# Kernel optimization log

Hardware: AMD Instinct MI355X
Metric: run time of the kernel (lower is better)

The kernel has to match this reference:

```python
import jax, jax.numpy as jnp
import numpy as np

B, CIN, W = 4, 3, 28          # batch, in_channels, image size (= max_pos_embedding)
MID, HEADS, G, COUT = 16, 8, 4, 64
HALF = MID // 2               # row / col embedding dims


def _embed(u, w1, b1, gamma, beta, w2, b2):
    """Positional-embedding MLP applied elementwise to scalars u (N,).
    Conv2d(1->16,k=1) -> LayerNorm(16 channels) -> Swish -> Conv2d(16->MID/2,k=1)."""
    h = u[:, None] * w1[None, :] + b1                     # (N, 16)
    mu = h.mean(-1, keepdims=True)
    var = ((h - mu) ** 2).mean(-1, keepdims=True)
    h = gamma * (h - mu) / jnp.sqrt(var + 1e-5) + beta    # LayerNorm over channels
    h = h * jax.nn.sigmoid(h)                             # Swish
    return h @ w2.T + b2                                  # (N, HALF)


def _rot_indices():
    """Acted relative-position lookup indices for the 4 rotations.
    Values index into u = concat(rel, -rel) where rel = linspace(-1,1,2W-1)."""
    n = 2 * W - 1
    ar = np.arange(W)
    rel = ar[None, :] - ar[:, None] + (W - 1)             # rel[i,k] in [0, 2W-2]
    R = np.broadcast_to(rel[:, None, :, None], (W,) * 4)  # depends on (i,k)
    C = np.broadcast_to(rel[None, :, None, :], (W,) * 4)  # depends on (j,l)
    # rotation by 0/90/180/270 deg acting on (row, col) relative coordinates
    ridx = np.stack([R, C + n, R + n, C], 0)              # row component index
    cidx = np.stack([C, R, C + n, R + n], 0)              # col component index
    return jnp.asarray(ridx, jnp.int32), jnp.asarray(cidx, jnp.int32)


def setup_inputs() -> dict:
    key = jax.random.key(0)
    ks = jax.random.split(key, 24)
    def nrm(k, shape, fan):
        return jax.random.normal(k, shape, jnp.float32) / np.float32(np.sqrt(fan))
    inp = {"x": jax.random.normal(ks[0], (B, CIN, W, W), jnp.float32)}
    inp["wq"] = nrm(ks[1], (MID * HEADS, CIN), CIN); inp["bq"] = jnp.zeros((MID * HEADS,), jnp.float32)
    inp["wk"] = nrm(ks[2], (MID * HEADS, CIN), CIN); inp["bk"] = jnp.zeros((MID * HEADS,), jnp.float32)
    inp["wv"] = nrm(ks[3], (MID * HEADS, CIN), CIN); inp["bv"] = jnp.zeros((MID * HEADS,), jnp.float32)
    inp["w_out"] = nrm(ks[4], (COUT, MID * HEADS), MID * HEADS); inp["b_out"] = jnp.zeros((COUT,), jnp.float32)
    for pfx, base in (("row", 5), ("col", 12)):
        inp[f"{pfx}_w1"] = nrm(ks[base], (16,), 1)
        inp[f"{pfx}_b1"] = jnp.zeros((16,), jnp.float32)
        inp[f"{pfx}_gamma"] = jnp.ones((16,), jnp.float32)
        inp[f"{pfx}_beta"] = jnp.zeros((16,), jnp.float32)
        inp[f"{pfx}_w2"] = nrm(ks[base + 1], (HALF, 16), 16)
        inp[f"{pfx}_b2"] = jnp.zeros((HALF,), jnp.float32)
    inp["ridx"], inp["cidx"] = _rot_indices()
    return inp


def reference(x, wq, bq, wk, bk, wv, bv, w_out, b_out,
              row_w1, row_b1, row_gamma, row_beta, row_w2, row_b2,
              col_w1, col_b1, col_gamma, col_beta, col_w2, col_b2,
              ridx, cidx):
    b, c, H, Wd = x.shape
    # 1x1-conv q/k/v, viewed as (b, mid, heads, H, W)
    q = (jnp.einsum('oc,bcij->boij', wq, x) + bq[:, None, None]).reshape(b, MID, HEADS, H, Wd)
    k_ = (jnp.einsum('oc,bcij->boij', wk, x) + bk[:, None, None]).reshape(b, MID, HEADS, H, Wd)
    v = (jnp.einsum('oc,bcij->boij', wv, x) + bv[:, None, None]).reshape(b, MID, HEADS, H, Wd)

    content = jnp.einsum('bmhij,bmhkl->bhijkl', q, k_)     # (b,h,i,j,k,l)

    lin = jnp.linspace(-1.0, 1.0, 2 * Wd - 1)
    u = jnp.concatenate([lin, -lin])                       # unique relative coords
    E_row = _embed(u, row_w1, row_b1, row_gamma, row_beta, row_w2, row_b2)
    E_col = _embed(u, col_w1, col_b1, col_gamma, col_beta, col_w2, col_b2)
    row_emb = E_row[ridx]                                  # (G,i,j,k,l,HALF)
    col_emb = E_col[cidx]

    scores = jnp.einsum('bmhij,gijklm->bhgijkl', q[:, :HALF], row_emb)
    scores = scores + jnp.einsum('bmhij,gijklm->bhgijkl', q[:, HALF:], col_emb)
    scores = (scores + content[:, :, None]) / np.float32(np.sqrt(c))

    sh = scores.shape                                      # softmax over flattened (k,l)
    probs = jax.nn.softmax(scores.reshape(sh[:-2] + (-1,)), axis=-1).reshape(sh)

    out_v = jnp.einsum('bhgijkl,bmhkl->bmhgij', probs, v)  # (b,mid,heads,G,i,j)
    out_v = out_v.reshape(b, MID * HEADS, G, H, Wd)
    out = jnp.einsum('om,bmgij->bogij', w_out, out_v) + b_out[:, None, None, None]
    return out
```

## Files before the change

kernel.cpp:

```cpp
#include <hip/hip_runtime.h>
#include <hip/hip_fp16.h>

#define NPOS 784
#define WDIM 28

typedef _Float16 f16x8 __attribute__((ext_vector_type(8)));
typedef _Float16 f16x4 __attribute__((ext_vector_type(4)));
typedef float    f32x4 __attribute__((ext_vector_type(4)));

__global__ __launch_bounds__(256) void prep_kernel(
    const float* __restrict__ x,
    const float* __restrict__ wk, const float* __restrict__ bk,
    const float* __restrict__ wv, const float* __restrict__ bv,
    const float* __restrict__ w_out,
    const float* __restrict__ rw1, const float* __restrict__ rb1,
    const float* __restrict__ rga, const float* __restrict__ rbe,
    const float* __restrict__ rw2, const float* __restrict__ rb2,
    const float* __restrict__ cw1, const float* __restrict__ cb1,
    const float* __restrict__ cga, const float* __restrict__ cbe,
    const float* __restrict__ cw2, const float* __restrict__ cb2,
    _Float16* __restrict__ Kfrag, _Float16* __restrict__ Vfrag,
    _Float16* __restrict__ Wfrag,
    float* __restrict__ Etr, float* __restrict__ Etc)
{
    const int t = threadIdx.x;
    if (blockIdx.x == 416) {
        int d = -1;
        const float *w1 = rw1, *b1 = rb1, *ga = rga, *be = rbe, *w2 = rw2, *b2 = rb2;
        float* E = Etr;
        if (t < 110) { d = t; }
        else if (t >= 128 && t < 238) { d = t - 128; w1 = cw1; b1 = cb1; ga = cga; be = cbe; w2 = cw2; b2 = cb2; E = Etc; }
        if (d < 0) return;
        float u = (d < 55) ? (-1.0f + (float)d * (2.0f / 54.0f))
                           : -(-1.0f + (float)(d - 55) * (2.0f / 54.0f));
        float hb[16], mu = 0.0f;
#pragma unroll
        for (int c = 0; c < 16; ++c) { hb[c] = u * w1[c] + b1[c]; mu += hb[c]; }
        mu *= (1.0f / 16.0f);
        float var = 0.0f;
#pragma unroll
        for (int c = 0; c < 16; ++c) { float dv = hb[c] - mu; var += dv * dv; }
        var *= (1.0f / 16.0f);
        float rstd = rsqrtf(var + 1e-5f);
#pragma unroll
        for (int c = 0; c < 16; ++c) {
            float hn = ga[c] * (hb[c] - mu) * rstd + be[c];
            hb[c] = hn / (1.0f + __expf(-hn));
        }
#pragma unroll
        for (int m = 0; m < 8; ++m) {
            float e = b2[m];
#pragma unroll
            for (int c = 0; c < 16; ++c) e += hb[c] * w2[m * 16 + c];
            E[m * 110 + d] = e;
        }
        return;
    }
    if (blockIdx.x == 417) {
        for (int idx = t; idx < 8192; idx += 256) {
            int obc = idx >> 9, lane = (idx >> 3) & 63, j = idx & 7;
            int o  = (obc >> 2) * 16 + (lane & 15);
            int mh = (obc & 3) * 32 + (lane >> 4) * 8 + j;
            Wfrag[idx] = (_Float16)w_out[o * 128 + mh];
        }
        return;
    }

    const int bid  = blockIdx.x;
    const int b    = bid / 104, rem = bid - b * 104;
    const int tile = rem >> 3, h = rem & 7;
    const int lane = t & 63, mg = t >> 6;
    const int bh   = b * 8 + h;

    {
        if (t < 128) {
            int sub = (t >> 5) & 3, l32 = 32 + (t & 31);
            int qz = tile * 4 + sub;
            if (qz < 49)
                *(f16x8*)(Kfrag + ((size_t)(bh * 49 + qz) * 64 + l32) * 8) = (f16x8){};
        }
        if (tile == 12 && t < 32)
            *(f16x8*)(Vfrag + ((size_t)(bh * 25 + 24) * 64 + 32 + t) * 8) = (f16x8){};
    }

    const int ij = tile * 64 + lane;
    if (ij >= NPOS) return;

    float x0 = x[(b * 3 + 0) * NPOS + ij];
    float x1 = x[(b * 3 + 1) * NPOS + ij];
    float x2 = x[(b * 3 + 2) * NPOS + ij];

    float4 kv;
    float vv[4];
#pragma unroll
    for (int j = 0; j < 4; ++j) {
        int m = mg * 4 + j, oc = m * 8 + h;
        float w0, w1, w2v;
        w0 = wk[oc*3+0]; w1 = wk[oc*3+1]; w2v = wk[oc*3+2];
        ((float*)&kv)[j] = bk[oc] + w0*x0 + w1*x1 + w2v*x2;
        w0 = wv[oc*3+0]; w1 = wv[oc*3+1]; w2v = wv[oc*3+2];
        vv[j] = bv[oc] + w0*x0 + w1*x1 + w2v*x2;
    }
    {
        int qt = ij >> 4;
        int lp = ((mg >> 1) << 4) | (ij & 15);
        int jb = (mg & 1) * 4;
        f16x4 k4 = {(_Float16)kv.x, (_Float16)kv.y, (_Float16)kv.z, (_Float16)kv.w};
        *(f16x4*)(Kfrag + ((size_t)(bh * 49 + qt) * 64 + lp) * 8 + jb) = k4;
    }
    {
        int s5 = ij >> 5, kk = ij & 31;
        _Float16* vb = Vfrag + (((size_t)(bh * 25 + s5) * 64 + ((kk >> 3) << 4)) << 3) + (kk & 7);
#pragma unroll
        for (int j = 0; j < 4; ++j) vb[(mg * 4 + j) * 8] = (_Float16)vv[j];
    }
}

#define UNI_OFF 56320
#define MX_OFF  97280
#define PS_OFF  98304
__global__ __launch_bounds__(1024, 1) void attn_kernel(
    const _Float16* __restrict__ Kfrag, const _Float16* __restrict__ Vfrag,
    const _Float16* __restrict__ Wfrag,
    const float* __restrict__ Etr, const float* __restrict__ Etc,
    const float* __restrict__ x,
    const float* __restrict__ wq, const float* __restrict__ bq,
    const float* __restrict__ b_out, float* __restrict__ out)
{
    __shared__ __align__(16) unsigned char smem[100352];
    const int t = threadIdx.x, wave = t >> 6, lane = t & 63;
    const int q15 = lane & 15, rg = lane >> 4;
    const int h = wave & 7, hf = wave >> 3;

    int bid = blockIdx.x;
    int xcd = bid & 7;
    int lb  = ((xcd < 4) ? xcd * 25 : 100 + (xcd - 4) * 24) + (bid >> 3);
    const int b = lb / 49, qt = lb - b * 49;
    const int bh = b * 8 + h;
    const int q_ij = qt * 16 + q15;
    const int iq = q_ij / WDIM, jq = q_ij % WDIM;
    const float scale = 0.57735026918962576f;

    float* ebuf = (float*)(smem + UNI_OFF);
    for (int i = t; i < 1760; i += 1024) ebuf[i] = (i < 880) ? Etr[i] : Etc[i - 880];

    float ql[8], qh[8];
    {
        float x0 = x[(b * 3 + 0) * NPOS + q_ij];
        float x1 = x[(b * 3 + 1) * NPOS + q_ij];
        float x2 = x[(b * 3 + 2) * NPOS + q_ij];
#pragma unroll
        for (int m = 0; m < 8; ++m) {
            int oc = m * 8 + h;
            ql[m] = bq[oc] + wq[oc*3+0]*x0 + wq[oc*3+1]*x1 + wq[oc*3+2]*x2;
        }
#pragma unroll
        for (int m = 0; m < 8; ++m) {
            int oc = (m + 8) * 8 + h;
            qh[m] = bq[oc] + wq[oc*3+0]*x0 + wq[oc*3+1]*x1 + wq[oc*3+2]*x2;
        }
    }
    f16x8 qf = {};
    if (rg == 0) {
#pragma unroll
        for (int j = 0; j < 8; ++j) qf[j] = (_Float16)ql[j];
    } else if (rg == 1) {
#pragma unroll
        for (int j = 0; j < 8; ++j) qf[j] = (_Float16)qh[j];
    }
    __syncthreads();

    {
        unsigned int* tab32 = (unsigned int*)smem + (h * 16 + q15) * 110;
        const int d5 = hf * 55;
        float m1 = -3.0e38f, m2 = -3.0e38f;
        for (int tv = 0; tv < 14; ++tv) {
            int dd = rg * 14 + tv;
            if (dd < 55) {
                float a1 = 0, a2 = 0;
#pragma unroll
                for (int mm = 0; mm < 8; ++mm) {
                    a1 += ql[mm] * ebuf[mm * 110 + dd + d5];
                    a2 += qh[mm] * ebuf[880 + mm * 110 + dd + d5];
                }
                m1 = fmaxf(m1, a1); m2 = fmaxf(m2, a2);
            }
        }
        m1 = fmaxf(m1, __shfl_xor(m1, 16, 64)); m1 = fmaxf(m1, __shfl_xor(m1, 32, 64));
        m2 = fmaxf(m2, __shfl_xor(m2, 16, 64)); m2 = fmaxf(m2, __shfl_xor(m2, 32, 64));
        for (int tv = 0; tv < 14; ++tv) {
            int dd = rg * 14 + tv;
            if (dd < 55) {
                float a1 = 0, a2 = 0;
#pragma unroll
                for (int mm = 0; mm < 8; ++mm) {
                    a1 += ql[mm] * ebuf[mm * 110 + dd + d5];
                    a2 += qh[mm] * ebuf[880 + mm * 110 + dd + d5];
                }
                __half2 hp = __floats2half2_rn(__expf(scale * (a1 - m1)),
                                               __expf(scale * (a2 - m2)));
                tab32[dd * 2 + hf] = *(unsigned int*)&hp;
            }
        }
    }
    __syncthreads();

    const f16x8* kchunk = (const f16x8*)(Kfrag + (size_t)bh * 49 * 64 * 8);

    float mx = -3.0e38f;
#pragma unroll 5
    for (int i = 0; i < 25; ++i) {
        int ch = 2 * i + hf;
        if (ch < 49) {
            f16x8 kf = kchunk[ch * 64 + lane];
            f32x4 s = __builtin_amdgcn_mfma_f32_16x16x32_f16(kf, qf, (f32x4){0,0,0,0}, 0, 0, 0);
            mx = fmaxf(mx, fmaxf(fmaxf(s[0], s[1]), fmaxf(s[2], s[3])));
        }
    }
    mx = fmaxf(mx, __shfl_xor(mx, 16, 64));
    mx = fmaxf(mx, __shfl_xor(mx, 32, 64));
    float* mxbuf = (float*)(smem + MX_OFF);
    if (rg == 0) mxbuf[wave * 16 + q15] = mx;
    __syncthreads();
    mx = fmaxf(mx, mxbuf[(wave ^ 8) * 16 + q15]);

    float ps0 = 0, ps1 = 0, ps2 = 0, ps3 = 0;
    f32x4 d0 = {0,0,0,0}, d1 = {0,0,0,0}, d2 = {0,0,0,0}, d3 = {0,0,0,0};
    _Float16* ptw = (_Float16*)(smem + UNI_OFF) + wave * 1280;
    const uint2* tab = (const uint2*)smem + (h * 16 + q15) * 55;
    const f16x8* vbase = (const f16x8*)(Vfrag + (size_t)bh * 25 * 64 * 8);
    const int wco = q15 * 40 + rg * 4;
    const int rco = (lane & 15) * 40 + (lane >> 4) * 8;

    int pv = hf;
    f16x8 kfA = kchunk[(2 * pv) * 64 + lane];
    f16x8 kfB = kchunk[(2 * pv + 1) * 64 + lane];
    f16x8 bf  = vbase[pv * 64 + lane];
    for (int i = 0; i < 13; ++i) {
        int pvn = pv + 2;
        int nA = (pvn * 2     < 49) ? pvn * 2     : 48;
        int nB = (pvn * 2 + 1 < 49) ? pvn * 2 + 1 : 48;
        int nV = (pvn < 25) ? pvn : 24;
        f16x8 kfA2 = kchunk[nA * 64 + lane];
        f16x8 kfB2 = kchunk[nB * 64 + lane];
        f16x8 bf2  = vbase[nV * 64 + lane];

        uint2 pk0[4], pk1[4];
#pragma unroll
        for (int c2 = 0; c2 < 2; ++c2) {
            int ch = pv * 2 + c2;
            uint2* pk = c2 ? pk1 : pk0;
            if (ch < 49) {
                f16x8 kf = c2 ? kfB : kfA;
                f32x4 s = __builtin_amdgcn_mfma_f32_16x16x32_f16(kf, qf, (f32x4){0,0,0,0}, 0, 0, 0);
                float pg[4][4];
#pragma unroll
                for (int reg = 0; reg < 4; ++reg) {
                    float ec = __expf((s[reg] - mx) * scale) * 64.0f;
                    int k = ch * 16 + rg * 4 + reg;
                    int rk = (k * 2341) >> 16;
                    int ck = k - rk * WDIM;
                    uint2 tr = tab[rk - iq + 27];
                    uint2 tc = tab[ck - jq + 27];
                    float2 r01 = __half22float2(*(__half2*)&tr.x);
                    float2 r23 = __half22float2(*(__half2*)&tr.y);
                    float2 c01 = __half22float2(*(__half2*)&tc.x);
                    float2 c23 = __half22float2(*(__half2*)&tc.y);
                    pg[0][reg] = ec * r01.x * c01.y;
                    pg[1][reg] = ec * r01.y * c23.x;
                    pg[2][reg] = ec * r23.x * c23.y;
                    pg[3][reg] = ec * r23.y * c01.x;
                    ps0 += pg[0][reg]; ps1 += pg[1][reg];
                    ps2 += pg[2][reg]; ps3 += pg[3][reg];
                }
#pragma unroll
                for (int g = 0; g < 4; ++g) {
                    __half2 a01 = __floats2half2_rn(pg[g][0], pg[g][1]);
                    __half2 a23 = __floats2half2_rn(pg[g][2], pg[g][3]);
                    pk[g].x = *(unsigned int*)&a01; pk[g].y = *(unsigned int*)&a23;
                }
            } else {
#pragma unroll
                for (int g = 0; g < 4; ++g) { pk[g].x = 0u; pk[g].y = 0u; }
            }
        }
        _Float16* b0 = ptw;
        _Float16* b1 = ptw + 640;
        *(uint2*)(b0 + wco) = pk0[0]; *(uint2*)(b0 + wco + 16) = pk1[0];
        *(uint2*)(b1 + wco) = pk0[1]; *(uint2*)(b1 + wco + 16) = pk1[1];
        { f16x8 a = *(const f16x8*)(b0 + rco);
          d0 = __builtin_amdgcn_mfma_f32_16x16x32_f16(a, bf, d0, 0, 0, 0); }
        *(uint2*)(b0 + wco) = pk0[2]; *(uint2*)(b0 + wco + 16) = pk1[2];
        { f16x8 a = *(const f16x8*)(b1 + rco);
          d1 = __builtin_amdgcn_mfma_f32_16x16x32_f16(a, bf, d1, 0, 0, 0); }
        *(uint2*)(b1 + wco) = pk0[3]; *(uint2*)(b1 + wco + 16) = pk1[3];
        { f16x8 a = *(const f16x8*)(b0 + rco);
          d2 = __builtin_amdgcn_mfma_f32_16x16x32_f16(a, bf, d2, 0, 0, 0); }
        { f16x8 a = *(const f16x8*)(b1 + rco);
          d3 = __builtin_amdgcn_mfma_f32_16x16x32_f16(a, bf, d3, 0, 0, 0); }
        kfA = kfA2; kfB = kfB2; bf = bf2; pv = pvn;
    }
    ps0 += __shfl_xor(ps0, 16, 64); ps0 += __shfl_xor(ps0, 32, 64);
    ps1 += __shfl_xor(ps1, 16, 64); ps1 += __shfl_xor(ps1, 32, 64);
    ps2 += __shfl_xor(ps2, 16, 64); ps2 += __shfl_xor(ps2, 32, 64);
    ps3 += __shfl_xor(ps3, 16, 64); ps3 += __shfl_xor(ps3, 32, 64);

    __syncthreads();
    float* dbuf = (float*)(smem + UNI_OFF);
    float* psb  = (float*)(smem + PS_OFF);
    if (hf) {
        float* ds = dbuf + (wave - 8) * (64 * 17) + lane * 17;
        ds[0]=d0[0];  ds[1]=d0[1];  ds[2]=d0[2];  ds[3]=d0[3];
        ds[4]=d1[0];  ds[5]=d1[1];  ds[6]=d1[2];  ds[7]=d1[3];
        ds[8]=d2[0];  ds[9]=d2[1];  ds[10]=d2[2]; ds[11]=d2[3];
        ds[12]=d3[0]; ds[13]=d3[1]; ds[14]=d3[2]; ds[15]=d3[3];
        if (rg == 0) {
            float* pp = psb + (wave - 8) * 64 + q15 * 4;
            pp[0] = ps0; pp[1] = ps1; pp[2] = ps2; pp[3] = ps3;
        }
    }
    __syncthreads();
    if (!hf) {
        const float* ds = dbuf + wave * (64 * 17) + lane * 17;
        d0[0]+=ds[0];  d0[1]+=ds[1];  d0[2]+=ds[2];  d0[3]+=ds[3];
        d1[0]+=ds[4];  d1[1]+=ds[5];  d1[2]+=ds[6];  d1[3]+=ds[7];
        d2[0]+=ds[8];  d2[1]+=ds[9];  d2[2]+=ds[10]; d2[3]+=ds[11];
        d3[0]+=ds[12]; d3[1]+=ds[13]; d3[2]+=ds[14]; d3[3]+=ds[15];
        const float* pp = psb + wave * 64 + q15 * 4;
        ps0 += pp[0]; ps1 += pp[1]; ps2 += pp[2]; ps3 += pp[3];
    }
    __syncthreads();
    _Float16* ovh = (_Float16*)(smem + UNI_OFF);
    if (!hf) {
        float i0 = 1.0f / ps0, i1 = 1.0f / ps1, i2 = 1.0f / ps2, i3 = 1.0f / ps3;
        int mo = q15 * 8 + h;
#pragma unroll
        for (int reg = 0; reg < 4; ++reg) {
            int q = rg * 4 + reg;
            ovh[(0*16 + q)*136 + mo] = (_Float16)(d0[reg] * __shfl(i0, q, 64));
            ovh[(1*16 + q)*136 + mo] = (_Float16)(d1[reg] * __shfl(i1, q, 64));
            ovh[(2*16 + q)*136 + mo] = (_Float16)(d2[reg] * __shfl(i2, q, 64));
            ovh[(3*16 + q)*136 + mo] = (_Float16)(d3[reg] * __shfl(i3, q, 64));
        }
    }
    __syncthreads();

    {
        int ob = wave >> 2, g = wave & 3;
        f32x4 dd = {0,0,0,0};
#pragma unroll
        for (int c = 0; c < 4; ++c) {
            f16x8 wa = *(const f16x8*)(Wfrag + ((size_t)((ob * 4 + c) * 64 + lane)) * 8);
            f16x8 vb = *(const f16x8*)(ovh + (g * 16 + q15) * 136 + c * 32 + rg * 8);
            dd = __builtin_amdgcn_mfma_f32_16x16x32_f16(wa, vb, dd, 0, 0, 0);
        }
#pragma unroll
        for (int reg = 0; reg < 4; ++reg) {
            int o = ob * 16 + rg * 4 + reg;
            out[((size_t)(b * 64 + o) * 4 + g) * NPOS + qt * 16 + q15] = dd[reg] + b_out[o];
        }
    }
}

extern "C" void kernel_launch(void* const* d_in, const int* in_sizes, int n_in,
                              void* d_out, int out_size, void* d_ws, size_t ws_size,
                              hipStream_t stream)
{
    const float* x     = (const float*)d_in[0];
    const float* wq    = (const float*)d_in[1];
    const float* bq    = (const float*)d_in[2];
    const float* wk    = (const float*)d_in[3];
    const float* bk    = (const float*)d_in[4];
    const float* wv    = (const float*)d_in[5];
    const float* bv    = (const float*)d_in[6];
    const float* w_out = (const float*)d_in[7];
    const float* b_out = (const float*)d_in[8];
    const float* rw1 = (const float*)d_in[9];
    const float* rb1 = (const float*)d_in[10];
    const float* rga = (const float*)d_in[11];
    const float* rbe = (const float*)d_in[12];
    const float* rw2 = (const float*)d_in[13];
    const float* rb2 = (const float*)d_in[14];
    const float* cw1 = (const float*)d_in[15];
    const float* cb1 = (const float*)d_in[16];
    const float* cga = (const float*)d_in[17];
    const float* cbe = (const float*)d_in[18];
    const float* cw2 = (const float*)d_in[19];
    const float* cb2 = (const float*)d_in[20];

    float* Etr       = (float*)d_ws;
    float* Etc       = Etr + 880;
    _Float16* Kfrag  = (_Float16*)(Etc + 880);
    _Float16* Vfrag  = Kfrag + 802816;
    _Float16* Wfrag  = Vfrag + 409600;

    prep_kernel<<<418, 256, 0, stream>>>(x, wk, bk, wv, bv, w_out,
                                         rw1, rb1, rga, rbe, rw2, rb2,
                                         cw1, cb1, cga, cbe, cw2, cb2,
                                         Kfrag, Vfrag, Wfrag, Etr, Etc);
    attn_kernel<<<196, 1024, 0, stream>>>(Kfrag, Vfrag, Wfrag, Etr, Etc,
                                          x, wq, bq, b_out, (float*)d_out);
}
```

Before: 161.4 us.

## Compute softmax row sums via ones-MFMA and restage probability tiles in LDS

The per-lane scalar probability sum accumulators and their cross-lane shuffles are replaced by extra MFMAs against a ones vector, so the normalisers come out of the matrix unit in the same layout as the output. The LDS staging is changed so that all four rotation tiles are written first and then read back together, instead of the old interleaved write/read reuse of two buffers. This allows eight back-to-back MFMAs per iteration, wrapped in raised wave priority. Exp is computed with exp2f and a folded scale and offset, and the launch bound and shared-memory size grow to hold the larger staging buffers. The cost is twice as many MFMAs and more LDS.

```diff
diff --git a/kernel.cpp b/kernel.cpp
--- a/kernel.cpp
+++ b/kernel.cpp
@@ -117,9 +117,9 @@
 }
 
 #define UNI_OFF 56320
-#define MX_OFF  97280
-#define PS_OFF  98304
-__global__ __launch_bounds__(1024, 1) void attn_kernel(
+#define DB_OFF  17408
+#define MX_OFF  141312
+__global__ __launch_bounds__(1024, 4) void attn_kernel(
     const _Float16* __restrict__ Kfrag, const _Float16* __restrict__ Vfrag,
     const _Float16* __restrict__ Wfrag,
     const float* __restrict__ Etr, const float* __restrict__ Etc,
@@ -127,7 +127,7 @@
     const float* __restrict__ wq, const float* __restrict__ bq,
     const float* __restrict__ b_out, float* __restrict__ out)
 {
-    __shared__ __align__(16) unsigned char smem[100352];
+    __shared__ __align__(16) unsigned char smem[142336];
     const int t = threadIdx.x, wave = t >> 6, lane = t & 63;
     const int q15 = lane & 15, rg = lane >> 4;
     const int h = wave & 7, hf = wave >> 3;
@@ -208,13 +208,15 @@
     const f16x8* kchunk = (const f16x8*)(Kfrag + (size_t)bh * 49 * 64 * 8);
 
     float mx = -3.0e38f;
-#pragma unroll 5
-    for (int i = 0; i < 25; ++i) {
-        int ch = 2 * i + hf;
-        if (ch < 49) {
-            f16x8 kf = kchunk[ch * 64 + lane];
-            f32x4 s = __builtin_amdgcn_mfma_f32_16x16x32_f16(kf, qf, (f32x4){0,0,0,0}, 0, 0, 0);
-            mx = fmaxf(mx, fmaxf(fmaxf(s[0], s[1]), fmaxf(s[2], s[3])));
+    for (int pv = hf; pv < 25; pv += 2) {
+#pragma unroll
+        for (int c2 = 0; c2 < 2; ++c2) {
+            int ch = 2 * pv + c2;
+            if (ch < 49) {
+                f16x8 kf = kchunk[ch * 64 + lane];
+                f32x4 s = __builtin_amdgcn_mfma_f32_16x16x32_f16(kf, qf, (f32x4){0,0,0,0}, 0, 0, 0);
+                mx = fmaxf(mx, fmaxf(fmaxf(s[0], s[1]), fmaxf(s[2], s[3])));
+            }
         }
     }
     mx = fmaxf(mx, __shfl_xor(mx, 16, 64));
@@ -223,40 +225,43 @@
     if (rg == 0) mxbuf[wave * 16 + q15] = mx;
     __syncthreads();
     mx = fmaxf(mx, mxbuf[(wave ^ 8) * 16 + q15]);
-
-    float ps0 = 0, ps1 = 0, ps2 = 0, ps3 = 0;
+    const float c1  = 0.57735026918962576f * 1.44269504088896341f;
+    const float c2f = 6.0f - mx * c1;
+
     f32x4 d0 = {0,0,0,0}, d1 = {0,0,0,0}, d2 = {0,0,0,0}, d3 = {0,0,0,0};
-    _Float16* ptw = (_Float16*)(smem + UNI_OFF) + wave * 1280;
+    f32x4 e0 = {0,0,0,0}, e1 = {0,0,0,0}, e2 = {0,0,0,0}, e3 = {0,0,0,0};
+    _Float16* ptw = (_Float16*)(smem + UNI_OFF) + (size_t)wave * 2592;
     const uint2* tab = (const uint2*)smem + (h * 16 + q15) * 55;
+    const int prow  = (q15 & 3) * 4;
+    const int tbase = (q15 >> 2) * 648;
+    const int rof   = q15 * 40 + rg * 8;
     const f16x8* vbase = (const f16x8*)(Vfrag + (size_t)bh * 25 * 64 * 8);
-    const int wco = q15 * 40 + rg * 4;
-    const int rco = (lane & 15) * 40 + (lane >> 4) * 8;
-
-    int pv = hf;
-    f16x8 kfA = kchunk[(2 * pv) * 64 + lane];
-    f16x8 kfB = kchunk[(2 * pv + 1) * 64 + lane];
-    f16x8 bf  = vbase[pv * 64 + lane];
-    for (int i = 0; i < 13; ++i) {
+    f16x8 onesB;
+#pragma unroll
+    for (int j = 0; j < 8; ++j) onesB[j] = (_Float16)1.0f;
+
+    f16x8 kfA = kchunk[(2 * hf) * 64 + lane];
+    f16x8 kfB = kchunk[(2 * hf + 1) * 64 + lane];
+    f16x8 bf  = vbase[hf * 64 + lane];
+    for (int pv = hf; pv < 25; pv += 2) {
         int pvn = pv + 2;
-        int nA = (pvn * 2     < 49) ? pvn * 2     : 48;
-        int nB = (pvn * 2 + 1 < 49) ? pvn * 2 + 1 : 48;
+        int nA = (2 * pvn     < 49) ? 2 * pvn     : 48;
+        int nB = (2 * pvn + 1 < 49) ? 2 * pvn + 1 : 48;
         int nV = (pvn < 25) ? pvn : 24;
         f16x8 kfA2 = kchunk[nA * 64 + lane];
         f16x8 kfB2 = kchunk[nB * 64 + lane];
         f16x8 bf2  = vbase[nV * 64 + lane];
-
-        uint2 pk0[4], pk1[4];
 #pragma unroll
         for (int c2 = 0; c2 < 2; ++c2) {
-            int ch = pv * 2 + c2;
-            uint2* pk = c2 ? pk1 : pk0;
+            int ch = 2 * pv + c2;
+            int cb = rg * 4 + c2 * 16;
             if (ch < 49) {
                 f16x8 kf = c2 ? kfB : kfA;
                 f32x4 s = __builtin_amdgcn_mfma_f32_16x16x32_f16(kf, qf, (f32x4){0,0,0,0}, 0, 0, 0);
                 float pg[4][4];
 #pragma unroll
                 for (int reg = 0; reg < 4; ++reg) {
-                    float ec = __expf((s[reg] - mx) * scale) * 64.0f;
+                    float ec = exp2f(s[reg] * c1 + c2f);
                     int k = ch * 16 + rg * 4 + reg;
                     int rk = (k * 2341) >> 16;
                     int ck = k - rk * WDIM;
@@ -270,77 +275,74 @@
                     pg[1][reg] = ec * r01.y * c23.x;
                     pg[2][reg] = ec * r23.x * c23.y;
                     pg[3][reg] = ec * r23.y * c01.x;
-                    ps0 += pg[0][reg]; ps1 += pg[1][reg];
-                    ps2 += pg[2][reg]; ps3 += pg[3][reg];
                 }
 #pragma unroll
                 for (int g = 0; g < 4; ++g) {
                     __half2 a01 = __floats2half2_rn(pg[g][0], pg[g][1]);
                     __half2 a23 = __floats2half2_rn(pg[g][2], pg[g][3]);
-                    pk[g].x = *(unsigned int*)&a01; pk[g].y = *(unsigned int*)&a23;
+                    uint2 w; w.x = *(unsigned int*)&a01; w.y = *(unsigned int*)&a23;
+                    *(uint2*)(ptw + tbase + (prow + g) * 40 + cb) = w;
                 }
             } else {
-#pragma unroll
-                for (int g = 0; g < 4; ++g) { pk[g].x = 0u; pk[g].y = 0u; }
+                uint2 w; w.x = 0u; w.y = 0u;
+#pragma unroll
+                for (int g = 0; g < 4; ++g)
+                    *(uint2*)(ptw + tbase + (prow + g) * 40 + cb) = w;
             }
         }
-        _Float16* b0 = ptw;
-        _Float16* b1 = ptw + 640;
-        *(uint2*)(b0 + wco) = pk0[0]; *(uint2*)(b0 + wco + 16) = pk1[0];
-        *(uint2*)(b1 + wco) = pk0[1]; *(uint2*)(b1 + wco + 16) = pk1[1];
-        { f16x8 a = *(const f16x8*)(b0 + rco);
-          d0 = __builtin_amdgcn_mfma_f32_16x16x32_f16(a, bf, d0, 0, 0, 0); }
-        *(uint2*)(b0 + wco) = pk0[2]; *(uint2*)(b0 + wco + 16) = pk1[2];
-        { f16x8 a = *(const f16x8*)(b1 + rco);
-          d1 = __builtin_amdgcn_mfma_f32_16x16x32_f16(a, bf, d1, 0, 0, 0); }
-        *(uint2*)(b1 + wco) = pk0[3]; *(uint2*)(b1 + wco + 16) = pk1[3];
-        { f16x8 a = *(const f16x8*)(b0 + rco);
-          d2 = __builtin_amdgcn_mfma_f32_16x16x32_f16(a, bf, d2, 0, 0, 0); }
-        { f16x8 a = *(const f16x8*)(b1 + rco);
-          d3 = __builtin_amdgcn_mfma_f32_16x16x32_f16(a, bf, d3, 0, 0, 0); }
-        kfA = kfA2; kfB = kfB2; bf = bf2; pv = pvn;
-    }
-    ps0 += __shfl_xor(ps0, 16, 64); ps0 += __shfl_xor(ps0, 32, 64);
-    ps1 += __shfl_xor(ps1, 16, 64); ps1 += __shfl_xor(ps1, 32, 64);
-    ps2 += __shfl_xor(ps2, 16, 64); ps2 += __shfl_xor(ps2, 32, 64);
-    ps3 += __shfl_xor(ps3, 16, 64); ps3 += __shfl_xor(ps3, 32, 64);
-
-    __syncthreads();
-    float* dbuf = (float*)(smem + UNI_OFF);
-    float* psb  = (float*)(smem + PS_OFF);
+        f16x8 aA = *(const f16x8*)(ptw + 0 * 648 + rof);
+        f16x8 aB = *(const f16x8*)(ptw + 1 * 648 + rof);
+        f16x8 aC = *(const f16x8*)(ptw + 2 * 648 + rof);
+        f16x8 aD = *(const f16x8*)(ptw + 3 * 648 + rof);
+        __builtin_amdgcn_s_setprio(1);
+        d0 = __builtin_amdgcn_mfma_f32_16x16x32_f16(aA, bf, d0, 0, 0, 0);
+        e0 = __builtin_amdgcn_mfma_f32_16x16x32_f16(aA, onesB, e0, 0, 0, 0);
+        d1 = __builtin_amdgcn_mfma_f32_16x16x32_f16(aB, bf, d1, 0, 0, 0);
+        e1 = __builtin_amdgcn_mfma_f32_16x16x32_f16(aB, onesB, e1, 0, 0, 0);
+        d2 = __builtin_amdgcn_mfma_f32_16x16x32_f16(aC, bf, d2, 0, 0, 0);
+        e2 = __builtin_amdgcn_mfma_f32_16x16x32_f16(aC, onesB, e2, 0, 0, 0);
+        d3 = __builtin_amdgcn_mfma_f32_16x16x32_f16(aD, bf, d3, 0, 0, 0);
+        e3 = __builtin_amdgcn_mfma_f32_16x16x32_f16(aD, onesB, e3, 0, 0, 0);
+        __builtin_amdgcn_s_setprio(0);
+        kfA = kfA2; kfB = kfB2; bf = bf2;
+    }
+
+    __syncthreads();
+    float* dbuf = (float*)(smem + UNI_OFF + DB_OFF);
     if (hf) {
-        float* ds = dbuf + (wave - 8) * (64 * 17) + lane * 17;
+        float* ds = dbuf + h * (64 * 33) + lane * 33;
         ds[0]=d0[0];  ds[1]=d0[1];  ds[2]=d0[2];  ds[3]=d0[3];
         ds[4]=d1[0];  ds[5]=d1[1];  ds[6]=d1[2];  ds[7]=d1[3];
         ds[8]=d2[0];  ds[9]=d2[1];  ds[10]=d2[2]; ds[11]=d2[3];
         ds[12]=d3[0]; ds[13]=d3[1]; ds[14]=d3[2]; ds[15]=d3[3];
-        if (rg == 0) {
-            float* pp = psb + (wave - 8) * 64 + q15 * 4;
-            pp[0] = ps0; pp[1] = ps1; pp[2] = ps2; pp[3] = ps3;
-        }
-    }
-    __syncthreads();
+        ds[16]=e0[0]; ds[17]=e0[1]; ds[18]=e0[2]; ds[19]=e0[3];
+        ds[20]=e1[0]; ds[21]=e1[1]; ds[22]=e1[2]; ds[23]=e1[3];
+        ds[24]=e2[0]; ds[25]=e2[1]; ds[26]=e2[2]; ds[27]=e2[3];
+        ds[28]=e3[0]; ds[29]=e3[1]; ds[30]=e3[2]; ds[31]=e3[3];
+    }
+    __syncthreads();
+    _Float16* ovh = (_Float16*)(smem + UNI_OFF);
     if (!hf) {
-        const float* ds = dbuf + wave * (64 * 17) + lane * 17;
+        const float* ds = dbuf + h * (64 * 33) + lane * 33;
         d0[0]+=ds[0];  d0[1]+=ds[1];  d0[2]+=ds[2];  d0[3]+=ds[3];
         d1[0]+=ds[4];  d1[1]+=ds[5];  d1[2]+=ds[6];  d1[3]+=ds[7];
         d2[0]+=ds[8];  d2[1]+=ds[9];  d2[2]+=ds[10]; d2[3]+=ds[11];
         d3[0]+=ds[12]; d3[1]+=ds[13]; d3[2]+=ds[14]; d3[3]+=ds[15];
-        const float* pp = psb + wave * 64 + q15 * 4;
-        ps0 += pp[0]; ps1 += pp[1]; ps2 += pp[2]; ps3 += pp[3];
-    }
-    __syncthreads();
-    _Float16* ovh = (_Float16*)(smem + UNI_OFF);
-    if (!hf) {
-        float i0 = 1.0f / ps0, i1 = 1.0f / ps1, i2 = 1.0f / ps2, i3 = 1.0f / ps3;
+        e0[0]+=ds[16]; e0[1]+=ds[17]; e0[2]+=ds[18]; e0[3]+=ds[19];
+        e1[0]+=ds[20]; e1[1]+=ds[21]; e1[2]+=ds[22]; e1[3]+=ds[23];
+        e2[0]+=ds[24]; e2[1]+=ds[25]; e2[2]+=ds[26]; e2[3]+=ds[27];
+        e3[0]+=ds[28]; e3[1]+=ds[29]; e3[2]+=ds[30]; e3[3]+=ds[31];
         int mo = q15 * 8 + h;
 #pragma unroll
         for (int reg = 0; reg < 4; ++reg) {
-            int q = rg * 4 + reg;
-            ovh[(0*16 + q)*136 + mo] = (_Float16)(d0[reg] * __shfl(i0, q, 64));
-            ovh[(1*16 + q)*136 + mo] = (_Float16)(d1[reg] * __shfl(i1, q, 64));
-            ovh[(2*16 + q)*136 + mo] = (_Float16)(d2[reg] * __shfl(i2, q, 64));
-            ovh[(3*16 + q)*136 + mo] = (_Float16)(d3[reg] * __shfl(i3, q, 64));
+            float i0 = (e0[reg] > 0.0f) ? 1.0f / e0[reg] : 0.0f;
+            float i1 = (e1[reg] > 0.0f) ? 1.0f / e1[reg] : 0.0f;
+            float i2 = (e2[reg] > 0.0f) ? 1.0f / e2[reg] : 0.0f;
+            float i3 = (e3[reg] > 0.0f) ? 1.0f / e3[reg] : 0.0f;
+            ovh[(reg * 16 +      rg) * 136 + mo] = (_Float16)(d0[reg] * i0);
+            ovh[(reg * 16 +  4 + rg) * 136 + mo] = (_Float16)(d1[reg] * i1);
+            ovh[(reg * 16 +  8 + rg) * 136 + mo] = (_Float16)(d2[reg] * i2);
+            ovh[(reg * 16 + 12 + rg) * 136 + mo] = (_Float16)(d3[reg] * i3);
         }
     }
     __syncthreads();
```

Measured after the change: 158.3 us. Within noise of the previous version (-1.9%).
